# Kernel tuning notes

Measured on AMD Instinct MI355X. Metric: run time of the kernel, lower is better.

## Reference

```python
import jax, jax.numpy as jnp
import numpy as np

N = 100000
E = 600000
F_IN = 128
HID = 256
C = 64


def setup_inputs() -> dict:
    key = jax.random.key(0)
    ks = jax.random.split(key, 6)
    x = jax.random.normal(ks[0], (N, F_IN), dtype=jnp.float32)
    edge_index = jax.random.randint(ks[1], (2, E), 0, N, dtype=jnp.int64)
    W1 = jax.random.normal(ks[2], (F_IN, HID), dtype=jnp.float32) * (1.0 / np.sqrt(F_IN))
    b1 = jnp.zeros((HID,), dtype=jnp.float32)
    W2 = jax.random.normal(ks[3], (HID, C), dtype=jnp.float32) * (1.0 / np.sqrt(HID))
    b2 = jnp.zeros((C,), dtype=jnp.float32)
    return {"x": x, "W1": W1, "b1": b1, "W2": W2, "b2": b2, "edge_index": edge_index}


def _gcn_conv(h, W, b, src, dst, norm, self_w):
    # h: [N, F_in] -> [N, F_out]; symmetric-normalized aggregation over A+I
    h = h @ W  # [N, F_out]
    agg = jax.ops.segment_sum(h[src] * norm[:, None], dst, num_segments=N)
    agg = agg + h * self_w[:, None]  # self-loop contribution d^{-1/2}*d^{-1/2}
    return agg + b


def reference(x, W1, b1, W2, b2, edge_index):
    src, dst = edge_index[0], edge_index[1]
    # degree of A + I (self-loops added): 1 + in-degree
    deg = jnp.ones((N,), dtype=x.dtype).at[dst].add(1.0)
    dinv = jax.lax.rsqrt(deg)
    norm = dinv[src] * dinv[dst]  # [E]
    self_w = dinv * dinv          # [N]

    h = _gcn_conv(x, W1, b1, src, dst, norm, self_w)
    h = jax.nn.relu(h)
    # dropout is identity in eval mode (training=False)
    out = _gcn_conv(h, W2, b2, src, dst, norm, self_w)
    return jax.nn.log_softmax(out, axis=1)
```

## Files before the change

kernel.cpp:

```cpp
#include <hip/hip_runtime.h>
#include <cstdint>
#include <cstddef>

#define N_NODES 100000
#define N_EDGES 600000
#define F_IN    128
#define HID     256
#define NC      64
#define NB_SCAN 391

typedef __attribute__((ext_vector_type(8))) short bf16x8;
typedef __attribute__((ext_vector_type(4))) float f32x4;

__device__ __forceinline__ unsigned short f2bf(float f) {
    unsigned int u = __float_as_uint(f);
    u = (u + 0x7FFFu + ((u >> 16) & 1u)) >> 16;
    return (unsigned short)u;
}
__device__ __forceinline__ float bf2f(unsigned short u) {
    return __uint_as_float(((unsigned int)u) << 16);
}

__device__ __forceinline__ int load_idx(const void* ei, int m, long long i) {
    return m ? (int)((const long long*)ei)[i] : ((const int*)ei)[i];
}

__global__ void k_hist(const void* __restrict__ ei, const int* __restrict__ mode,
                       int* __restrict__ deg) {
    int e = blockIdx.x * blockDim.x + threadIdx.x;
    if (e >= N_EDGES) return;
    int d = load_idx(ei, *mode, (long long)N_EDGES + e);
    atomicAdd(&deg[d], 1);
}

__global__ void k_scanA(const int* __restrict__ deg, int* __restrict__ ptmp,
                        int* __restrict__ bsum) {
    __shared__ int sm[256];
    int i = blockIdx.x * 256 + threadIdx.x;
    int v = (i < N_NODES) ? deg[i] : 0;
    sm[threadIdx.x] = v;
    __syncthreads();
    for (int off = 1; off < 256; off <<= 1) {
        int t = (threadIdx.x >= off) ? sm[threadIdx.x - off] : 0;
        __syncthreads();
        sm[threadIdx.x] += t;
        __syncthreads();
    }
    if (i < N_NODES) ptmp[i] = sm[threadIdx.x] - v;
    if (threadIdx.x == 255) bsum[blockIdx.x] = sm[255];
}

__global__ void k_scanB(int* __restrict__ bsum) {
    __shared__ int sm[512];
    int i = threadIdx.x;
    int v = (i < NB_SCAN) ? bsum[i] : 0;
    sm[i] = v;
    __syncthreads();
    for (int off = 1; off < 512; off <<= 1) {
        int t = (i >= off) ? sm[i - off] : 0;
        __syncthreads();
        sm[i] += t;
        __syncthreads();
    }
    if (i < NB_SCAN) bsum[i] = sm[i] - v;
}

__global__ void k_scanC(const int* __restrict__ deg, const int* __restrict__ ptmp,
                        const int* __restrict__ bsum, int* __restrict__ row_ptr,
                        int* __restrict__ cursor, float* __restrict__ dinv) {
    int i = blockIdx.x * 256 + threadIdx.x;
    if (i < N_NODES) {
        int rp = ptmp[i] + bsum[blockIdx.x];
        row_ptr[i] = rp;
        cursor[i]  = rp;
        dinv[i]    = rsqrtf(1.0f + (float)deg[i]);
    }
    if (i == 0) row_ptr[N_NODES] = N_EDGES;
}

__global__ void k_fill(const void* __restrict__ ei, const int* __restrict__ mode,
                       int* __restrict__ cursor, int* __restrict__ csr_src) {
    int e = blockIdx.x * blockDim.x + threadIdx.x;
    if (e >= N_EDGES) return;
    int m = *mode;
    int s = load_idx(ei, m, e);
    int d = load_idx(ei, m, (long long)N_EDGES + e);
    int pos = atomicAdd(&cursor[d], 1);
    csr_src[pos] = s;
}

#define XB_BLOCKS (N_NODES * F_IN / 8 / 256)
#define W1_BLOCKS (F_IN * HID / 256)
#define W2_BLOCKS (HID * NC / 256)
#define PREP_BLOCKS (XB_BLOCKS + W1_BLOCKS + W2_BLOCKS)
__global__ void k_prep(const float* __restrict__ x, const float* __restrict__ W1,
                       const float* __restrict__ W2, unsigned short* __restrict__ xbf,
                       unsigned short* __restrict__ W1T, unsigned short* __restrict__ W2T,
                       int* __restrict__ deg, const int* __restrict__ ei_words,
                       int* __restrict__ mode) {
    int bid = blockIdx.x;
    int tid = threadIdx.x;
    if (bid < XB_BLOCKS) {
        int i = bid * 256 + tid;
        const float4* xr = (const float4*)x;
        float4 a = xr[(size_t)i * 2];
        float4 b = xr[(size_t)i * 2 + 1];
        bf16x8 o;
        o[0] = (short)f2bf(a.x); o[1] = (short)f2bf(a.y);
        o[2] = (short)f2bf(a.z); o[3] = (short)f2bf(a.w);
        o[4] = (short)f2bf(b.x); o[5] = (short)f2bf(b.y);
        o[6] = (short)f2bf(b.z); o[7] = (short)f2bf(b.w);
        *(bf16x8*)(xbf + (size_t)i * 8) = o;
    } else if (bid < XB_BLOCKS + W1_BLOCKS) {
        int i = (bid - XB_BLOCKS) * 256 + tid;
        int k = i >> 8, n = i & 255;
        W1T[n * F_IN + k] = f2bf(W1[i]);
    } else if (bid < PREP_BLOCKS) {
        int i = (bid - XB_BLOCKS - W1_BLOCKS) * 256 + tid;
        int k = i >> 6, n = i & 63;
        W2T[n * HID + k] = f2bf(W2[i]);
    } else if (bid < PREP_BLOCKS + NB_SCAN) {
        int i = (bid - PREP_BLOCKS) * 256 + tid;
        if (i < N_NODES) deg[i] = 0;
    } else {
        if (tid == 0) {
            int allz = 1;
            for (int i = 0; i < 64; ++i) {
                long long s = (long long)i * (N_EDGES - 1) / 63;
                if (ei_words[2 * s + 1] != 0) { allz = 0; break; }
            }
            *mode = allz;
        }
    }
}

__global__ __launch_bounds__(256) void k_mlp_fused(
        const unsigned short* __restrict__ xbf, const int* __restrict__ row_ptr,
        const int* __restrict__ csr_src, const float* __restrict__ dinv,
        const unsigned short* __restrict__ W1T, const float* __restrict__ b1,
        const unsigned short* __restrict__ W2T, unsigned short* __restrict__ hx2) {
    __shared__ unsigned short px_lds[32 * F_IN];
    __shared__ unsigned short hlds[32 * HID];
    const int lane = threadIdx.x & 63;
    const int w    = threadIdx.x >> 6;
    const int l15  = lane & 15, lhi = lane >> 4;
    const int row0 = blockIdx.x * 32;

    {
        const int r   = threadIdx.x >> 3;
        const int seg = threadIdx.x & 7;
        const int n   = row0 + r;
        const float dn = dinv[n];
        float acc16[16];
        const unsigned short* xp = xbf + (size_t)n * F_IN + seg * 16;
        bf16x8 v0 = *(const bf16x8*)(xp);
        bf16x8 v1 = *(const bf16x8*)(xp + 8);
#pragma unroll
        for (int t = 0; t < 8; ++t) {
            acc16[t]     = bf2f((unsigned short)v0[t]) * dn;
            acc16[8 + t] = bf2f((unsigned short)v1[t]) * dn;
        }
        int e0 = row_ptr[n], e1 = row_ptr[n + 1];
        float wvN = 0.f; bf16x8 u0N, u1N;
        if (e0 < e1) {
            int s0 = csr_src[e0];
            wvN = dinv[s0];
            const unsigned short* sp = xbf + (size_t)s0 * F_IN + seg * 16;
            u0N = *(const bf16x8*)(sp);
            u1N = *(const bf16x8*)(sp + 8);
        }
        for (int k = e0; k < e1; ++k) {
            float wv = wvN; bf16x8 u0 = u0N, u1 = u1N;
            if (k + 1 < e1) {
                int s2 = csr_src[k + 1];
                wvN = dinv[s2];
                const unsigned short* sp = xbf + (size_t)s2 * F_IN + seg * 16;
                u0N = *(const bf16x8*)(sp);
                u1N = *(const bf16x8*)(sp + 8);
            }
#pragma unroll
            for (int t = 0; t < 8; ++t) {
                acc16[t]     = fmaf(bf2f((unsigned short)u0[t]), wv, acc16[t]);
                acc16[8 + t] = fmaf(bf2f((unsigned short)u1[t]), wv, acc16[8 + t]);
            }
        }
        bf16x8 w0, w1;
#pragma unroll
        for (int t = 0; t < 8; ++t) {
            w0[t] = (short)f2bf(acc16[t] * dn);
            w1[t] = (short)f2bf(acc16[8 + t] * dn);
        }
        unsigned base = (unsigned)(r * 256 + seg * 32);
        unsigned sw   = (unsigned)((r & 7) << 4);
        *(bf16x8*)((char*)px_lds + ((base) ^ sw))      = w0;
        *(bf16x8*)((char*)px_lds + ((base + 16) ^ sw)) = w1;
    }
    __syncthreads();

    {
        const int col0 = w * 64;
        bf16x8 a[4][2];
#pragma unroll
        for (int ks = 0; ks < 4; ++ks)
#pragma unroll
            for (int mt = 0; mt < 2; ++mt) {
                unsigned byte = (unsigned)((mt * 16 + l15) * 256 + ks * 64 + lhi * 16)
                              ^ (unsigned)((l15 & 7) << 4);
                a[ks][mt] = *(const bf16x8*)((const char*)px_lds + byte);
            }

        f32x4 acc[2][4];
#pragma unroll
        for (int mt = 0; mt < 2; ++mt)
#pragma unroll
            for (int nt = 0; nt < 4; ++nt) acc[mt][nt] = (f32x4){0.f, 0.f, 0.f, 0.f};

#pragma unroll
        for (int ks = 0; ks < 4; ++ks) {
#pragma unroll
            for (int nt = 0; nt < 4; ++nt) {
                bf16x8 b = *(const bf16x8*)(W1T + (size_t)(col0 + nt * 16 + l15) * F_IN + ks * 32 + lhi * 8);
#pragma unroll
                for (int mt = 0; mt < 2; ++mt)
                    acc[mt][nt] = __builtin_amdgcn_mfma_f32_16x16x32_bf16(b, a[ks][mt], acc[mt][nt], 0, 0, 0);
            }
        }

#pragma unroll
        for (int mt = 0; mt < 2; ++mt) {
            const int lr = mt * 16 + l15;
#pragma unroll
            for (int nt = 0; nt < 4; ++nt) {
                int c0 = col0 + nt * 16 + lhi * 4;
                float4 bb = *(const float4*)(b1 + c0);
                ushort4 o;
                o.x = f2bf(fmaxf(acc[mt][nt][0] + bb.x, 0.f));
                o.y = f2bf(fmaxf(acc[mt][nt][1] + bb.y, 0.f));
                o.z = f2bf(fmaxf(acc[mt][nt][2] + bb.z, 0.f));
                o.w = f2bf(fmaxf(acc[mt][nt][3] + bb.w, 0.f));
                unsigned byte = (unsigned)(lr * (HID * 2) + c0 * 2) ^ ((lr & 7) << 4);
                *(ushort4*)((char*)hlds + byte) = o;
            }
        }
    }
    __syncthreads();

    {
        const int lr = (w & 1) * 16 + l15;
        const int cb = (w >> 1) * 32;
        bf16x8 a2[8];
#pragma unroll
        for (int ks = 0; ks < 8; ++ks) {
            unsigned byte = (unsigned)(lr * (HID * 2) + ks * 64 + lhi * 16) ^ ((lr & 7) << 4);
            a2[ks] = *(const bf16x8*)((const char*)hlds + byte);
        }
        f32x4 acc2[2];
#pragma unroll
        for (int nt = 0; nt < 2; ++nt) acc2[nt] = (f32x4){0.f, 0.f, 0.f, 0.f};
#pragma unroll
        for (int nt = 0; nt < 2; ++nt) {
            const unsigned short* pb = W2T + (size_t)(cb + nt * 16 + l15) * HID + lhi * 8;
#pragma unroll
            for (int ks = 0; ks < 8; ++ks) {
                bf16x8 b = *(const bf16x8*)(pb + ks * 32);
                acc2[nt] = __builtin_amdgcn_mfma_f32_16x16x32_bf16(b, a2[ks], acc2[nt], 0, 0, 0);
            }
        }
        const int r = row0 + lr;
#pragma unroll
        for (int nt = 0; nt < 2; ++nt) {
            int c0 = cb + nt * 16 + lhi * 4;
            ushort4 o;
            o.x = f2bf(acc2[nt][0]); o.y = f2bf(acc2[nt][1]);
            o.z = f2bf(acc2[nt][2]); o.w = f2bf(acc2[nt][3]);
            *(ushort4*)(hx2 + (size_t)r * NC + c0) = o;
        }
    }
}

__global__ void k_gather2sm(const unsigned short* __restrict__ hx2,
                            const int* __restrict__ row_ptr,
                            const int* __restrict__ csr_src, const float* __restrict__ dinv,
                            const float* __restrict__ b2, float* __restrict__ out) {
    int g = threadIdx.x >> 4;
    int j = threadIdx.x & 15;
    int n = blockIdx.x * 16 + g;
    float dn = dinv[n];
    ushort4 sv = *(const ushort4*)(hx2 + (size_t)n * NC + j * 4);
    float ax = bf2f(sv.x) * dn, ay = bf2f(sv.y) * dn,
          az = bf2f(sv.z) * dn, aw = bf2f(sv.w) * dn;
    int e0 = row_ptr[n], e1 = row_ptr[n + 1];
    float wvN = 0.f; ushort4 vN;
    if (e0 < e1) {
        int s0 = csr_src[e0];
        wvN = dinv[s0];
        vN = *(const ushort4*)(hx2 + (size_t)s0 * NC + j * 4);
    }
    for (int k = e0; k < e1; ++k) {
        float wv = wvN; ushort4 v = vN;
        if (k + 1 < e1) {
            int s2 = csr_src[k + 1];
            wvN = dinv[s2];
            vN = *(const ushort4*)(hx2 + (size_t)s2 * NC + j * 4);
        }
        ax = fmaf(bf2f(v.x), wv, ax); ay = fmaf(bf2f(v.y), wv, ay);
        az = fmaf(bf2f(v.z), wv, az); aw = fmaf(bf2f(v.w), wv, aw);
    }
    const float4 b = ((const float4*)b2)[j];
    float4 o;
    o.x = fmaf(ax, dn, b.x); o.y = fmaf(ay, dn, b.y);
    o.z = fmaf(az, dn, b.z); o.w = fmaf(aw, dn, b.w);
    float mx = fmaxf(fmaxf(o.x, o.y), fmaxf(o.z, o.w));
#pragma unroll
    for (int msk = 8; msk; msk >>= 1) mx = fmaxf(mx, __shfl_xor(mx, msk));
    float s4 = expf(o.x - mx) + expf(o.y - mx) + expf(o.z - mx) + expf(o.w - mx);
#pragma unroll
    for (int msk = 8; msk; msk >>= 1) s4 += __shfl_xor(s4, msk);
    float ls = mx + logf(s4);
    o.x -= ls; o.y -= ls; o.z -= ls; o.w -= ls;
    ((float4*)out)[(size_t)n * 16 + j] = o;
}

extern "C" void kernel_launch(void* const* d_in, const int* in_sizes, int n_in,
                              void* d_out, int out_size, void* d_ws, size_t ws_size,
                              hipStream_t stream) {
    const float* x  = (const float*)d_in[0];
    const float* W1 = (const float*)d_in[1];
    const float* b1 = (const float*)d_in[2];
    const float* W2 = (const float*)d_in[3];
    const float* b2 = (const float*)d_in[4];
    const void*  ei = d_in[5];
    float* out = (float*)d_out;

    char* ws = (char*)d_ws;
    size_t off = 0;
    auto alloc = [&](size_t bytes) {
        char* p = ws + off;
        off += (bytes + 255) & ~(size_t)255;
        return p;
    };
    int*            mode    = (int*)            alloc(4);
    int*            deg     = (int*)            alloc((size_t)N_NODES * 4);
    int*            ptmp    = (int*)            alloc((size_t)N_NODES * 4);
    int*            bsum    = (int*)            alloc(4096);
    int*            row_ptr = (int*)            alloc((size_t)(N_NODES + 1) * 4);
    int*            cursor  = (int*)            alloc((size_t)N_NODES * 4);
    float*          dinv    = (float*)          alloc((size_t)N_NODES * 4);
    int*            csr_src = (int*)            alloc((size_t)N_EDGES * 4);
    unsigned short* W1T     = (unsigned short*) alloc((size_t)F_IN * HID * 2);
    unsigned short* W2T     = (unsigned short*) alloc((size_t)HID * NC * 2);
    unsigned short* xbf     = (unsigned short*) alloc((size_t)N_NODES * F_IN * 2);
    unsigned short* hx2     = (unsigned short*) alloc((size_t)(N_NODES + 64) * NC * 2);

    k_prep<<<PREP_BLOCKS + NB_SCAN + 1, 256, 0, stream>>>(x, W1, W2, xbf, W1T, W2T,
                                                          deg, (const int*)ei, mode);

    k_hist<<<(N_EDGES + 255) / 256, 256, 0, stream>>>(ei, mode, deg);
    k_scanA<<<NB_SCAN, 256, 0, stream>>>(deg, ptmp, bsum);
    k_scanB<<<1, 512, 0, stream>>>(bsum);
    k_scanC<<<NB_SCAN, 256, 0, stream>>>(deg, ptmp, bsum, row_ptr, cursor, dinv);
    k_fill<<<(N_EDGES + 255) / 256, 256, 0, stream>>>(ei, mode, cursor, csr_src);

    k_mlp_fused<<<N_NODES / 32, 256, 0, stream>>>(xbf, row_ptr, csr_src, dinv,
                                                  W1T, b1, W2T, hx2);
    k_gather2sm<<<N_NODES / 16, 256, 0, stream>>>(hx2, row_ptr, csr_src, dinv, b2, out);
}
```

Baseline: 193.0 us.

## Double k_mlp_fused tile to 64 rows with 512 threads, drop gather prefetch

The fused aggregate+MLP kernel now handles 64 rows per block with 8 waves instead of 32 rows with 4 waves. Each W1T/W2T slice is loaded once per block for twice as many rows, and the per-block overhead is spread over more work. Bounds checks are added for the partial final tile. The software prefetch of the next neighbor in the gather loop is removed, which simplifies the loop but may expose more load latency. The larger LDS footprint per block (48 KB) may lower the number of resident blocks.

Result: slower. 205.2 us (+6.3%).

```diff
diff --git a/kernel.cpp b/kernel.cpp
--- a/kernel.cpp
+++ b/kernel.cpp
@@ -134,78 +134,71 @@
     }
 }
 
-__global__ __launch_bounds__(256) void k_mlp_fused(
+__global__ __launch_bounds__(512) void k_mlp_fused(
         const unsigned short* __restrict__ xbf, const int* __restrict__ row_ptr,
         const int* __restrict__ csr_src, const float* __restrict__ dinv,
         const unsigned short* __restrict__ W1T, const float* __restrict__ b1,
         const unsigned short* __restrict__ W2T, unsigned short* __restrict__ hx2) {
-    __shared__ unsigned short px_lds[32 * F_IN];
-    __shared__ unsigned short hlds[32 * HID];
+    __shared__ unsigned short px_lds[64 * F_IN];
+    __shared__ unsigned short hlds[64 * HID];
     const int lane = threadIdx.x & 63;
     const int w    = threadIdx.x >> 6;
     const int l15  = lane & 15, lhi = lane >> 4;
-    const int row0 = blockIdx.x * 32;
+    const int row0 = blockIdx.x * 64;
 
     {
         const int r   = threadIdx.x >> 3;
         const int seg = threadIdx.x & 7;
         const int n   = row0 + r;
-        const float dn = dinv[n];
-        float acc16[16];
-        const unsigned short* xp = xbf + (size_t)n * F_IN + seg * 16;
-        bf16x8 v0 = *(const bf16x8*)(xp);
-        bf16x8 v1 = *(const bf16x8*)(xp + 8);
-#pragma unroll
-        for (int t = 0; t < 8; ++t) {
-            acc16[t]     = bf2f((unsigned short)v0[t]) * dn;
-            acc16[8 + t] = bf2f((unsigned short)v1[t]) * dn;
-        }
-        int e0 = row_ptr[n], e1 = row_ptr[n + 1];
-        float wvN = 0.f; bf16x8 u0N, u1N;
-        if (e0 < e1) {
-            int s0 = csr_src[e0];
-            wvN = dinv[s0];
-            const unsigned short* sp = xbf + (size_t)s0 * F_IN + seg * 16;
-            u0N = *(const bf16x8*)(sp);
-            u1N = *(const bf16x8*)(sp + 8);
-        }
-        for (int k = e0; k < e1; ++k) {
-            float wv = wvN; bf16x8 u0 = u0N, u1 = u1N;
-            if (k + 1 < e1) {
-                int s2 = csr_src[k + 1];
-                wvN = dinv[s2];
-                const unsigned short* sp = xbf + (size_t)s2 * F_IN + seg * 16;
-                u0N = *(const bf16x8*)(sp);
-                u1N = *(const bf16x8*)(sp + 8);
-            }
+        if (n < N_NODES) {
+            const float dn = dinv[n];
+            float acc16[16];
+            const unsigned short* xp = xbf + (size_t)n * F_IN + seg * 16;
+            bf16x8 v0 = *(const bf16x8*)(xp);
+            bf16x8 v1 = *(const bf16x8*)(xp + 8);
 #pragma unroll
             for (int t = 0; t < 8; ++t) {
-                acc16[t]     = fmaf(bf2f((unsigned short)u0[t]), wv, acc16[t]);
-                acc16[8 + t] = fmaf(bf2f((unsigned short)u1[t]), wv, acc16[8 + t]);
-            }
-        }
-        bf16x8 w0, w1;
-#pragma unroll
-        for (int t = 0; t < 8; ++t) {
-            w0[t] = (short)f2bf(acc16[t] * dn);
-            w1[t] = (short)f2bf(acc16[8 + t] * dn);
-        }
-        unsigned base = (unsigned)(r * 256 + seg * 32);
-        unsigned sw   = (unsigned)((r & 7) << 4);
-        *(bf16x8*)((char*)px_lds + ((base) ^ sw))      = w0;
-        *(bf16x8*)((char*)px_lds + ((base + 16) ^ sw)) = w1;
+                acc16[t]     = bf2f((unsigned short)v0[t]) * dn;
+                acc16[8 + t] = bf2f((unsigned short)v1[t]) * dn;
+            }
+            int e0 = row_ptr[n], e1 = row_ptr[n + 1];
+            for (int k = e0; k < e1; ++k) {
+                int s = csr_src[k];
+                float wv = dinv[s];
+                const unsigned short* sp = xbf + (size_t)s * F_IN + seg * 16;
+                bf16x8 u0 = *(const bf16x8*)(sp);
+                bf16x8 u1 = *(const bf16x8*)(sp + 8);
+#pragma unroll
+                for (int t = 0; t < 8; ++t) {
+                    acc16[t]     = fmaf(bf2f((unsigned short)u0[t]), wv, acc16[t]);
+                    acc16[8 + t] = fmaf(bf2f((unsigned short)u1[t]), wv, acc16[8 + t]);
+                }
+            }
+            bf16x8 w0, w1;
+#pragma unroll
+            for (int t = 0; t < 8; ++t) {
+                w0[t] = (short)f2bf(acc16[t] * dn);
+                w1[t] = (short)f2bf(acc16[8 + t] * dn);
+            }
+            unsigned base = (unsigned)(r * 256 + seg * 32);
+            unsigned sw   = (unsigned)((r & 7) << 4);
+            *(bf16x8*)((char*)px_lds + ((base) ^ sw))      = w0;
+            *(bf16x8*)((char*)px_lds + ((base + 16) ^ sw)) = w1;
+        }
     }
     __syncthreads();
 
     {
-        const int col0 = w * 64;
+        const int rl0  = (w >> 2) * 32;
+        const int col0 = (w & 3) * 64;
         bf16x8 a[4][2];
 #pragma unroll
         for (int ks = 0; ks < 4; ++ks)
 #pragma unroll
             for (int mt = 0; mt < 2; ++mt) {
-                unsigned byte = (unsigned)((mt * 16 + l15) * 256 + ks * 64 + lhi * 16)
-                              ^ (unsigned)((l15 & 7) << 4);
+                const int lr = rl0 + mt * 16 + l15;
+                unsigned byte = (unsigned)(lr * 256 + ks * 64 + lhi * 16)
+                              ^ (unsigned)((lr & 7) << 4);
                 a[ks][mt] = *(const bf16x8*)((const char*)px_lds + byte);
             }
 
@@ -228,7 +221,7 @@
 
 #pragma unroll
         for (int mt = 0; mt < 2; ++mt) {
-            const int lr = mt * 16 + l15;
+            const int lr = rl0 + mt * 16 + l15;
 #pragma unroll
             for (int nt = 0; nt < 4; ++nt) {
                 int c0 = col0 + nt * 16 + lhi * 4;
@@ -246,8 +239,8 @@
     __syncthreads();
 
     {
-        const int lr = (w & 1) * 16 + l15;
-        const int cb = (w >> 1) * 32;
+        const int lr = (w >> 1) * 16 + l15;
+        const int cb = (w & 1) * 32;
         bf16x8 a2[8];
 #pragma unroll
         for (int ks = 0; ks < 8; ++ks) {
@@ -267,13 +260,15 @@
             }
         }
         const int r = row0 + lr;
-#pragma unroll
-        for (int nt = 0; nt < 2; ++nt) {
-            int c0 = cb + nt * 16 + lhi * 4;
-            ushort4 o;
-            o.x = f2bf(acc2[nt][0]); o.y = f2bf(acc2[nt][1]);
-            o.z = f2bf(acc2[nt][2]); o.w = f2bf(acc2[nt][3]);
-            *(ushort4*)(hx2 + (size_t)r * NC + c0) = o;
+        if (r < N_NODES) {
+#pragma unroll
+            for (int nt = 0; nt < 2; ++nt) {
+                int c0 = cb + nt * 16 + lhi * 4;
+                ushort4 o;
+                o.x = f2bf(acc2[nt][0]); o.y = f2bf(acc2[nt][1]);
+                o.z = f2bf(acc2[nt][2]); o.w = f2bf(acc2[nt][3]);
+                *(ushort4*)(hx2 + (size_t)r * NC + c0) = o;
+            }
         }
     }
 }
@@ -361,7 +356,7 @@
     k_scanC<<<NB_SCAN, 256, 0, stream>>>(deg, ptmp, bsum, row_ptr, cursor, dinv);
     k_fill<<<(N_EDGES + 255) / 256, 256, 0, stream>>>(ei, mode, cursor, csr_src);
 
-    k_mlp_fused<<<N_NODES / 32, 256, 0, stream>>>(xbf, row_ptr, csr_src, dinv,
-                                                  W1T, b1, W2T, hx2);
+    k_mlp_fused<<<(N_NODES + 63) / 64, 512, 0, stream>>>(xbf, row_ptr, csr_src, dinv,
+                                                         W1T, b1, W2T, hx2);
     k_gather2sm<<<N_NODES / 16, 256, 0, stream>>>(hx2, row_ptr, csr_src, dinv, b2, out);
 }
```
